# Optimization experiments

Measured on AMD Instinct MI355X. Metric: run time of the kernel, lower is better.

## Reference

```python
import jax, jax.numpy as jnp
import numpy as np

B, N, E = 64, 256, 2048          # graphs per batch, nodes per subgraph, edges per subgraph
V, D, H = 50000, 128, 4          # vocab_size, hidden_dim, heads
NEG_SLOPE = 0.2                  # PyG GATConv default LeakyReLU slope


def setup_inputs() -> dict:
    key = jax.random.key(0)
    ks = jax.random.split(key, 16)
    s = 0.05
    return {
        "neighbors_node1": jax.random.randint(ks[0], (B, N), 0, V),
        "neighbors_node2": jax.random.randint(ks[1], (B, N), 0, V),
        "adj1": jax.random.randint(ks[2], (B, 2, E), 0, N),
        "adj2": jax.random.randint(ks[3], (B, 2, E), 0, N),
        "emb": jax.random.normal(ks[4], (V + 1, D), jnp.float32) * 0.02,
        # GATConv 1: lin weight [H*D, D], att_src/att_dst [H, D], bias [D] (concat=False)
        "W1": jax.random.normal(ks[5], (H * D, D), jnp.float32) * s,
        "att_src1": jax.random.normal(ks[6], (H, D), jnp.float32) * s,
        "att_dst1": jax.random.normal(ks[7], (H, D), jnp.float32) * s,
        "b1": jnp.zeros((D,), jnp.float32),
        # GATConv 2
        "W2": jax.random.normal(ks[8], (H * D, D), jnp.float32) * s,
        "att_src2": jax.random.normal(ks[9], (H, D), jnp.float32) * s,
        "att_dst2": jax.random.normal(ks[10], (H, D), jnp.float32) * s,
        "b2": jnp.zeros((D,), jnp.float32),
        # final MLP: Linear(2D -> 1)
        "mlp_w": jax.random.normal(ks[11], (1, 2 * D), jnp.float32) * s,
        "mlp_b": jnp.zeros((1,), jnp.float32),
    }


def _gat_conv(x, edge_index, W, a_src, a_dst, bias):
    """PyG GATConv, concat=False (mean over heads), with self-loops.
    x: [N, D] node features; edge_index: [2, E] (row=src j, col=dst i)."""
    xh = (x @ W.T).reshape(N, H, D)                      # [N, H, D]
    loop = jnp.arange(N)
    src = jnp.concatenate([edge_index[0], loop])          # [E+N]
    dst = jnp.concatenate([edge_index[1], loop])
    asrc = jnp.einsum('nhd,hd->nh', xh, a_src)            # [N, H]
    adst = jnp.einsum('nhd,hd->nh', xh, a_dst)
    e = jax.nn.leaky_relu(asrc[src] + adst[dst], NEG_SLOPE)   # [E+N, H]
    # softmax over incoming edges of each dst node
    m = jax.ops.segment_max(e, dst, num_segments=N)
    ex = jnp.exp(e - m[dst])
    denom = jax.ops.segment_sum(ex, dst, num_segments=N)
    alpha = ex / denom[dst]                               # [E+N, H]
    out = jax.ops.segment_sum(xh[src] * alpha[:, :, None], dst, num_segments=N)  # [N, H, D]
    return out.mean(axis=1) + bias                        # [N, D]


def reference(neighbors_node1, neighbors_node2, adj1, adj2, emb,
              W1, att_src1, att_dst1, b1,
              W2, att_src2, att_dst2, b2,
              mlp_w, mlp_b):
    f1 = jax.vmap(lambda n, ei: _gat_conv(emb[n], ei, W1, att_src1, att_dst1, b1))(
        neighbors_node1, adj1)                            # [B, N, D]
    f2 = jax.vmap(lambda n, ei: _gat_conv(emb[n], ei, W2, att_src2, att_dst2, b2))(
        neighbors_node2, adj2)
    feats = jnp.concatenate([f1[:, 0], f2[:, 0]], axis=-1)  # center node of each subgraph -> [B, 2D]
    return (feats @ mlp_w.T + mlp_b)[:, 0]                # [B]
```

## Files before the change

kernel.cpp:

```cpp
#include <hip/hip_runtime.h>
#include <hip/hip_bf16.h>

#define Bg 64
#define Nn 256
#define Ee 2048
#define Dd 128
#define Hh 4
#define MAXJ 40
#define RS 132

__device__ __forceinline__ float loadf(const void* p, long i, int f32) {
    return f32 ? ((const float*)p)[i]
               : __bfloat162float(((const __hip_bfloat16*)p)[i]);
}

__global__ __launch_bounds__(128) void precompute_kernel(
    const void* W1, const void* as1, const void* ad1, const void* b1,
    const void* W2, const void* as2, const void* ad2, const void* b2,
    const void* mlpw, const void* mlpb, float* wv)
{
    __shared__ float s_av[Dd];
    __shared__ float s_red[128];
    __shared__ int   s_f32;
    const int k = threadIdx.x;
    const int r = blockIdx.x;

    if (k == 0) s_f32 = 0;
    __syncthreads();
    {
        float v = __bfloat162float(((const __hip_bfloat16*)W1)[k]);
        if (!(v > -64.f && v < 64.f)) atomicOr(&s_f32, 1);
    }
    __syncthreads();
    const int f32 = s_f32;

    if (r < 24) {
        const int h = r & 3;
        const int t = (r >> 2) % 3;
        const int l = r / 12;
        const void* avp; long off;
        if (t == 0)      { avp = l ? as2 : as1; off = (long)h * Dd; }
        else if (t == 1) { avp = l ? ad2 : ad1; off = (long)h * Dd; }
        else             { avp = mlpw;          off = (long)l * Dd; }
        s_av[k] = loadf(avp, off + k, f32);
        __syncthreads();

        const void* W = l ? W2 : W1;
        float acc = 0.f;
        if (f32) {
            const float* Wf = (const float*)W + (long)h * Dd * Dd + k;
            #pragma unroll 8
            for (int d = 0; d < Dd; ++d) acc += s_av[d] * Wf[(long)d * Dd];
        } else {
            const __hip_bfloat16* Wb =
                (const __hip_bfloat16*)W + (long)h * Dd * Dd + k;
            #pragma unroll 8
            for (int d = 0; d < Dd; ++d)
                acc += s_av[d] * __bfloat162float(Wb[(long)d * Dd]);
        }
        wv[r * Dd + k] = acc;
    } else {
        const int l = r - 24;
        s_red[k] = loadf(l ? b2 : b1, k, f32) * loadf(mlpw, (long)l * Dd + k, f32);
        __syncthreads();
        for (int s = 64; s > 0; s >>= 1) {
            if (k < s) s_red[k] += s_red[k + s];
            __syncthreads();
        }
        if (k == 0) {
            float a = s_red[0];
            if (l == 0) a += loadf(mlpb, 0, f32);
            wv[3072 + l] = a;
        }
    }
}

__global__ __launch_bounds__(256) void gat_main_kernel(
    const int* nn1, const int* nn2, const int* adj1, const int* adj2,
    const void* emb, const void* W1, const float* wv, void* out)
{
    __shared__ float s_wv[24 * RS];
    __shared__ float s_rows[2 * MAXJ * RS];
    __shared__ float s_bdot[2];
    __shared__ int   s_srcj[2][MAXJ];
    __shared__ int   s_gid[2 * MAXJ];
    __shared__ int   s_cnt[2];
    __shared__ int   s_f32;
    __shared__ float s_ps[2 * MAXJ * Hh], s_pm[2 * MAXJ * Hh];
    __shared__ float s_pd[2 * Hh], s_hval[2 * Hh];

    const int tid = threadIdx.x;
    const int b = blockIdx.x;

    if (tid == 0) { s_f32 = 0; s_cnt[0] = 0; s_cnt[1] = 0; }
    __syncthreads();

    {
        float v = __bfloat162float(((const __hip_bfloat16*)W1)[tid]);
        if (!(v > -64.f && v < 64.f)) atomicOr(&s_f32, 1);
    }
    for (int i = tid; i < 768; i += 256) {
        float4 f = ((const float4*)wv)[i];
        int el = i * 4, row = el >> 7, k = el & 127;
        *(float4*)&s_wv[row * RS + k] = f;
    }
    if (tid < 2) s_bdot[tid] = wv[3072 + tid];
    for (int v = tid; v < 2 * (Ee / 4); v += 256) {
        int l = v >> 9, i = v & 511;
        const int* adj = (l ? adj2 : adj1) + (long)b * 2 * Ee;
        int4 d4 = ((const int4*)(adj + Ee))[i];
        int base = i * 4;
        if (d4.x == 0) { int p = atomicAdd(&s_cnt[l], 1); if (p < MAXJ - 1) s_srcj[l][p] = adj[base + 0]; }
        if (d4.y == 0) { int p = atomicAdd(&s_cnt[l], 1); if (p < MAXJ - 1) s_srcj[l][p] = adj[base + 1]; }
        if (d4.z == 0) { int p = atomicAdd(&s_cnt[l], 1); if (p < MAXJ - 1) s_srcj[l][p] = adj[base + 2]; }
        if (d4.w == 0) { int p = atomicAdd(&s_cnt[l], 1); if (p < MAXJ - 1) s_srcj[l][p] = adj[base + 3]; }
    }
    __syncthreads();
    const int f32 = s_f32;
    if (tid < 2) {
        int c = s_cnt[tid];
        if (c > MAXJ - 1) c = MAXJ - 1;
        s_srcj[tid][c] = 0;
        s_cnt[tid] = c + 1;
    }
    __syncthreads();
    const int cnt0 = s_cnt[0], cnt1 = s_cnt[1];
    const int tot = cnt0 + cnt1;

    if (tid < 2 * MAXJ) {
        int l = tid / MAXJ, j = tid % MAXJ;
        int cl = l ? cnt1 : cnt0;
        if (j < cl) {
            const int* nodes = l ? nn2 : nn1;
            s_gid[l ? (cnt0 + j) : j] = nodes[b * Nn + s_srcj[l][j]];
        }
    }
    __syncthreads();

    for (int idx = tid; idx < tot * 32; idx += 256) {
        int j = idx >> 5, k4 = (idx & 31) * 4;
        long gid = s_gid[j];
        float4 f;
        if (f32) {
            f = ((const float4*)emb)[gid * 32 + (k4 >> 2)];
        } else {
            const __hip_bfloat16* e = (const __hip_bfloat16*)emb + gid * Dd + k4;
            f.x = __bfloat162float(e[0]); f.y = __bfloat162float(e[1]);
            f.z = __bfloat162float(e[2]); f.w = __bfloat162float(e[3]);
        }
        *(float4*)&s_rows[j * RS + k4] = f;
    }
    __syncthreads();

    int ntask = tot * 8 + 8;
    for (int task = tid; task < ntask; task += 256) {
        int j, h, t, l;
        if (task < tot * 8) {
            j = task >> 3; h = (task >> 1) & 3; t = (task & 1) ? 2 : 0;
            l = (j < cnt0) ? 0 : 1;
        } else {
            int z = task - tot * 8;
            l = z >> 2; h = z & 3; t = 1;
            j = l ? (cnt0 + cnt1 - 1) : (cnt0 - 1);
        }
        const float* wrow = s_wv + ((l * 3 + t) * 4 + h) * RS;
        const float* row  = s_rows + j * RS;
        float acc = 0.f;
        #pragma unroll 8
        for (int k = 0; k < Dd; ++k) acc += row[k] * wrow[k];
        if (task < tot * 8) {
            if (task & 1) s_pm[j * Hh + h] = acc;
            else          s_ps[j * Hh + h] = acc;
        } else {
            s_pd[(l << 2) | h] = acc;
        }
    }
    __syncthreads();

    if (tid < 8) {
        int l = tid >> 2, h = tid & 3;
        int j0 = l ? cnt0 : 0;
        int j1 = l ? (cnt0 + cnt1) : cnt0;
        float pd = s_pd[tid], m = -1e30f;
        for (int j = j0; j < j1; ++j) {
            float e = s_ps[j * Hh + h] + pd;
            e = (e >= 0.f) ? e : 0.2f * e;
            s_ps[j * Hh + h] = e;
            if (e > m) m = e;
        }
        float den = 0.f, num = 0.f;
        for (int j = j0; j < j1; ++j) {
            float ex = expf(s_ps[j * Hh + h] - m);
            den += ex;
            num += ex * s_pm[j * Hh + h];
        }
        s_hval[tid] = num / den;
    }
    __syncthreads();
    if (tid == 0) {
        float r = 0.25f * (s_hval[0] + s_hval[1] + s_hval[2] + s_hval[3]) + s_bdot[0]
                + 0.25f * (s_hval[4] + s_hval[5] + s_hval[6] + s_hval[7]) + s_bdot[1];
        if (f32) ((float*)out)[b] = r;
        else     ((__hip_bfloat16*)out)[b] = __float2bfloat16(r);
    }
}

extern "C" void kernel_launch(void* const* d_in, const int* in_sizes, int n_in,
                              void* d_out, int out_size, void* d_ws, size_t ws_size,
                              hipStream_t stream) {
    const int* nn1  = (const int*)d_in[0];
    const int* nn2  = (const int*)d_in[1];
    const int* adj1 = (const int*)d_in[2];
    const int* adj2 = (const int*)d_in[3];
    float* wv = (float*)d_ws;

    precompute_kernel<<<26, 128, 0, stream>>>(
        d_in[5],   d_in[6],   d_in[7],
        d_in[8],
        d_in[9],   d_in[10],  d_in[11],
        d_in[12],
        d_in[13],  d_in[14],  wv);

    gat_main_kernel<<<Bg, 256, 0, stream>>>(
        nn1, nn2, adj1, adj2, d_in[4] , d_in[5] , wv, d_out);
}
```

Measured before the change: 112.3 us.

## Fuse weight-vector precompute into main GAT kernel, drop separate launch

Removes the separate precompute kernel. Each of the 64 blocks now computes the attention- and MLP-projected weight vectors (W^T·a for src, dst and mlp, per head and layer) plus the bias dot products directly into shared memory. This cuts one kernel launch and the global-memory round trip through the workspace. In exchange, every block redundantly reads both 256KB weight matrices and does the matrix-vector products itself. Embedding and attention-vector loads also switch to vectorized ushort4 reads with a bit-shift bf16 conversion.

```diff
diff --git a/kernel.cpp b/kernel.cpp
--- a/kernel.cpp
+++ b/kernel.cpp
@@ -9,85 +9,26 @@
 #define MAXJ 40
 #define RS 132
 
-__device__ __forceinline__ float loadf(const void* p, long i, int f32) {
-    return f32 ? ((const float*)p)[i]
-               : __bfloat162float(((const __hip_bfloat16*)p)[i]);
+__device__ __forceinline__ float bf2f(unsigned short u) {
+    return __uint_as_float(((unsigned)u) << 16);
 }
 
-__global__ __launch_bounds__(128) void precompute_kernel(
+__global__ __launch_bounds__(256) void gat_fused_kernel(
+    const int* nn1, const int* nn2, const int* adj1, const int* adj2,
+    const void* emb,
     const void* W1, const void* as1, const void* ad1, const void* b1,
     const void* W2, const void* as2, const void* ad2, const void* b2,
-    const void* mlpw, const void* mlpb, float* wv)
-{
-    __shared__ float s_av[Dd];
-    __shared__ float s_red[128];
-    __shared__ int   s_f32;
-    const int k = threadIdx.x;
-    const int r = blockIdx.x;
-
-    if (k == 0) s_f32 = 0;
-    __syncthreads();
-    {
-        float v = __bfloat162float(((const __hip_bfloat16*)W1)[k]);
-        if (!(v > -64.f && v < 64.f)) atomicOr(&s_f32, 1);
-    }
-    __syncthreads();
-    const int f32 = s_f32;
-
-    if (r < 24) {
-        const int h = r & 3;
-        const int t = (r >> 2) % 3;
-        const int l = r / 12;
-        const void* avp; long off;
-        if (t == 0)      { avp = l ? as2 : as1; off = (long)h * Dd; }
-        else if (t == 1) { avp = l ? ad2 : ad1; off = (long)h * Dd; }
-        else             { avp = mlpw;          off = (long)l * Dd; }
-        s_av[k] = loadf(avp, off + k, f32);
-        __syncthreads();
-
-        const void* W = l ? W2 : W1;
-        float acc = 0.f;
-        if (f32) {
-            const float* Wf = (const float*)W + (long)h * Dd * Dd + k;
-            #pragma unroll 8
-            for (int d = 0; d < Dd; ++d) acc += s_av[d] * Wf[(long)d * Dd];
-        } else {
-            const __hip_bfloat16* Wb =
-                (const __hip_bfloat16*)W + (long)h * Dd * Dd + k;
-            #pragma unroll 8
-            for (int d = 0; d < Dd; ++d)
-                acc += s_av[d] * __bfloat162float(Wb[(long)d * Dd]);
-        }
-        wv[r * Dd + k] = acc;
-    } else {
-        const int l = r - 24;
-        s_red[k] = loadf(l ? b2 : b1, k, f32) * loadf(mlpw, (long)l * Dd + k, f32);
-        __syncthreads();
-        for (int s = 64; s > 0; s >>= 1) {
-            if (k < s) s_red[k] += s_red[k + s];
-            __syncthreads();
-        }
-        if (k == 0) {
-            float a = s_red[0];
-            if (l == 0) a += loadf(mlpb, 0, f32);
-            wv[3072 + l] = a;
-        }
-    }
-}
-
-__global__ __launch_bounds__(256) void gat_main_kernel(
-    const int* nn1, const int* nn2, const int* adj1, const int* adj2,
-    const void* emb, const void* W1, const float* wv, void* out)
+    const void* mlpw, const void* mlpb, void* out)
 {
     __shared__ float s_wv[24 * RS];
     __shared__ float s_rows[2 * MAXJ * RS];
-    __shared__ float s_bdot[2];
+    __shared__ float s_red[256];
     __shared__ int   s_srcj[2][MAXJ];
     __shared__ int   s_gid[2 * MAXJ];
     __shared__ int   s_cnt[2];
     __shared__ int   s_f32;
     __shared__ float s_ps[2 * MAXJ * Hh], s_pm[2 * MAXJ * Hh];
-    __shared__ float s_pd[2 * Hh], s_hval[2 * Hh];
+    __shared__ float s_pd[2 * Hh], s_hval[2 * Hh], s_bdot[2];
 
     const int tid = threadIdx.x;
     const int b = blockIdx.x;
@@ -99,25 +40,100 @@
         float v = __bfloat162float(((const __hip_bfloat16*)W1)[tid]);
         if (!(v > -64.f && v < 64.f)) atomicOr(&s_f32, 1);
     }
-    for (int i = tid; i < 768; i += 256) {
-        float4 f = ((const float4*)wv)[i];
-        int el = i * 4, row = el >> 7, k = el & 127;
-        *(float4*)&s_wv[row * RS + k] = f;
-    }
-    if (tid < 2) s_bdot[tid] = wv[3072 + tid];
+    __syncthreads();
+    const int f32 = s_f32;
+
     for (int v = tid; v < 2 * (Ee / 4); v += 256) {
         int l = v >> 9, i = v & 511;
-        const int* adj = (l ? adj2 : adj1) + (long)b * 2 * Ee;
-        int4 d4 = ((const int4*)(adj + Ee))[i];
+        const int* adjp = (l ? adj2 : adj1) + (long)b * 2 * Ee;
+        int4 d4 = ((const int4*)(adjp + Ee))[i];
         int base = i * 4;
-        if (d4.x == 0) { int p = atomicAdd(&s_cnt[l], 1); if (p < MAXJ - 1) s_srcj[l][p] = adj[base + 0]; }
-        if (d4.y == 0) { int p = atomicAdd(&s_cnt[l], 1); if (p < MAXJ - 1) s_srcj[l][p] = adj[base + 1]; }
-        if (d4.z == 0) { int p = atomicAdd(&s_cnt[l], 1); if (p < MAXJ - 1) s_srcj[l][p] = adj[base + 2]; }
-        if (d4.w == 0) { int p = atomicAdd(&s_cnt[l], 1); if (p < MAXJ - 1) s_srcj[l][p] = adj[base + 3]; }
-    }
-    __syncthreads();
-    const int f32 = s_f32;
+        if (d4.x == 0) { int p = atomicAdd(&s_cnt[l], 1); if (p < MAXJ - 1) s_srcj[l][p] = adjp[base + 0]; }
+        if (d4.y == 0) { int p = atomicAdd(&s_cnt[l], 1); if (p < MAXJ - 1) s_srcj[l][p] = adjp[base + 1]; }
+        if (d4.z == 0) { int p = atomicAdd(&s_cnt[l], 1); if (p < MAXJ - 1) s_srcj[l][p] = adjp[base + 2]; }
+        if (d4.w == 0) { int p = atomicAdd(&s_cnt[l], 1); if (p < MAXJ - 1) s_srcj[l][p] = adjp[base + 3]; }
+    }
+
+    {
+        const int k = tid & 127;
+        const int g = tid >> 7;
+        for (int l = 0; l < 2; ++l) {
+            const void* W   = l ? W2 : W1;
+            const void* asp = l ? as2 : as1;
+            const void* adp = l ? ad2 : ad1;
+            for (int hh = 0; hh < 2; ++hh) {
+                const int h = g + 2 * hh;
+                float a0 = 0.f, a1 = 0.f, a2 = 0.f;
+                if (f32) {
+                    const float*  Wf = (const float*)W + (long)h * Dd * Dd + k;
+                    const float4* p0 = (const float4*)((const float*)asp + h * Dd);
+                    const float4* p1 = (const float4*)((const float*)adp + h * Dd);
+                    const float4* p2 = (const float4*)((const float*)mlpw + l * Dd);
+                    #pragma unroll 4
+                    for (int c = 0; c < 32; ++c) {
+                        float4 v0 = p0[c], v1 = p1[c], v2 = p2[c];
+                        float w0 = Wf[(4 * c + 0) * Dd];
+                        float w1 = Wf[(4 * c + 1) * Dd];
+                        float w2 = Wf[(4 * c + 2) * Dd];
+                        float w3 = Wf[(4 * c + 3) * Dd];
+                        a0 += v0.x * w0 + v0.y * w1 + v0.z * w2 + v0.w * w3;
+                        a1 += v1.x * w0 + v1.y * w1 + v1.z * w2 + v1.w * w3;
+                        a2 += v2.x * w0 + v2.y * w1 + v2.z * w2 + v2.w * w3;
+                    }
+                } else {
+                    const __hip_bfloat16* Wb =
+                        (const __hip_bfloat16*)W + (long)h * Dd * Dd + k;
+                    const ushort* q0 = (const ushort*)asp + h * Dd;
+                    const ushort* q1 = (const ushort*)adp + h * Dd;
+                    const ushort* q2 = (const ushort*)mlpw + l * Dd;
+                    #pragma unroll 4
+                    for (int c = 0; c < 32; ++c) {
+                        ushort4 u0 = *(const ushort4*)(q0 + 4 * c);
+                        ushort4 u1 = *(const ushort4*)(q1 + 4 * c);
+                        ushort4 u2 = *(const ushort4*)(q2 + 4 * c);
+                        float w0 = __bfloat162float(Wb[(4 * c + 0) * Dd]);
+                        float w1 = __bfloat162float(Wb[(4 * c + 1) * Dd]);
+                        float w2 = __bfloat162float(Wb[(4 * c + 2) * Dd]);
+                        float w3 = __bfloat162float(Wb[(4 * c + 3) * Dd]);
+                        a0 += bf2f(u0.x) * w0 + bf2f(u0.y) * w1 + bf2f(u0.z) * w2 + bf2f(u0.w) * w3;
+                        a1 += bf2f(u1.x) * w0 + bf2f(u1.y) * w1 + bf2f(u1.z) * w2 + bf2f(u1.w) * w3;
+                        a2 += bf2f(u2.x) * w0 + bf2f(u2.y) * w1 + bf2f(u2.z) * w2 + bf2f(u2.w) * w3;
+                    }
+                }
+                s_wv[((l * 3 + 0) * 4 + h) * RS + k] = a0;
+                s_wv[((l * 3 + 1) * 4 + h) * RS + k] = a1;
+                s_wv[((l * 3 + 2) * 4 + h) * RS + k] = a2;
+            }
+        }
+    }
+
+    {
+        int l = tid >> 7, d = tid & 127;
+        const void* bias = l ? b2 : b1;
+        float bv, mv;
+        if (f32) {
+            bv = ((const float*)bias)[d];
+            mv = ((const float*)mlpw)[l * Dd + d];
+        } else {
+            bv = __bfloat162float(((const __hip_bfloat16*)bias)[d]);
+            mv = __bfloat162float(((const __hip_bfloat16*)mlpw)[l * Dd + d]);
+        }
+        s_red[tid] = bv * mv;
+    }
+    __syncthreads();
+
+    for (int s = 64; s > 0; s >>= 1) {
+        if ((tid & 127) < s) s_red[tid] += s_red[tid + s];
+        __syncthreads();
+    }
     if (tid < 2) {
+        float a = s_red[tid * 128];
+        if (tid == 0) {
+            float mb = f32 ? ((const float*)mlpb)[0]
+                           : __bfloat162float(((const __hip_bfloat16*)mlpb)[0]);
+            a += mb;
+        }
+        s_bdot[tid] = a;
         int c = s_cnt[tid];
         if (c > MAXJ - 1) c = MAXJ - 1;
         s_srcj[tid][c] = 0;
@@ -144,9 +160,8 @@
         if (f32) {
             f = ((const float4*)emb)[gid * 32 + (k4 >> 2)];
         } else {
-            const __hip_bfloat16* e = (const __hip_bfloat16*)emb + gid * Dd + k4;
-            f.x = __bfloat162float(e[0]); f.y = __bfloat162float(e[1]);
-            f.z = __bfloat162float(e[2]); f.w = __bfloat162float(e[3]);
+            ushort4 u = *(const ushort4*)((const ushort*)emb + gid * Dd + k4);
+            f.x = bf2f(u.x); f.y = bf2f(u.y); f.z = bf2f(u.z); f.w = bf2f(u.w);
         }
         *(float4*)&s_rows[j * RS + k4] = f;
     }
@@ -161,7 +176,7 @@
         } else {
             int z = task - tot * 8;
             l = z >> 2; h = z & 3; t = 1;
-            j = l ? (cnt0 + cnt1 - 1) : (cnt0 - 1);
+            j = l ? (tot - 1) : (cnt0 - 1);
         }
         const float* wrow = s_wv + ((l * 3 + t) * 4 + h) * RS;
         const float* row  = s_rows + j * RS;
@@ -180,7 +195,7 @@
     if (tid < 8) {
         int l = tid >> 2, h = tid & 3;
         int j0 = l ? cnt0 : 0;
-        int j1 = l ? (cnt0 + cnt1) : cnt0;
+        int j1 = l ? tot : cnt0;
         float pd = s_pd[tid], m = -1e30f;
         for (int j = j0; j < j1; ++j) {
             float e = s_ps[j * Hh + h] + pd;
@@ -212,15 +227,14 @@
     const int* nn2  = (const int*)d_in[1];
     const int* adj1 = (const int*)d_in[2];
     const int* adj2 = (const int*)d_in[3];
-    float* wv = (float*)d_ws;
-
-    precompute_kernel<<<26, 128, 0, stream>>>(
+
+    gat_fused_kernel<<<Bg, 256, 0, stream>>>(
+        nn1, nn2, adj1, adj2,
+        d_in[4],
         d_in[5],   d_in[6],   d_in[7],
         d_in[8],
         d_in[9],   d_in[10],  d_in[11],
         d_in[12],
-        d_in[13],  d_in[14],  wv);
-
-    gat_main_kernel<<<Bg, 256, 0, stream>>>(
-        nn1, nn2, adj1, adj2, d_in[4] , d_in[5] , wv, d_out);
+        d_in[13],  d_in[14],
+        d_out);
 }
```

Result: slower. 118.4 us (+5.4%).
